# Kernel optimization log

Hardware: AMD Instinct MI355X
Metric: run time of the kernel (lower is better)

The kernel has to match this reference:

```python
import jax, jax.numpy as jnp
import numpy as np

# ---- module hyperparameters (from init_kwargs) ----
DIST = 25
N_IN, N_HID, N_OUT = 16, 128, 2
D_MODEL, D_STATE, D_CONV, EXPAND, HEADDIM = 256, 64, 4, 2, 64
D_INNER = EXPAND * D_MODEL            # 512
NHEADS = D_INNER // HEADDIM           # 8
CONV_DIM = D_INNER + 2 * D_STATE      # 640 (x, B, C share the conv)
D_IN_PROJ = 2 * D_INNER + 2 * D_STATE + NHEADS  # 1160
NUM_CHECK = DIST ** 2 - 1             # 624 (mamba seq len)
NPG = NUM_CHECK + DIST ** 2           # 1249 nodes per graph
BATCH = 64
N_NODES = BATCH * NPG                 # 79936
N_EDGES = N_NODES * 8                 # 639488


def setup_inputs() -> dict:
    key = jax.random.key(0)
    ks = jax.random.split(key, 16)
    w = lambda k, shape, s=0.02: jax.random.normal(k, shape, jnp.float32) * s
    return {
        "node_inputs": jax.random.normal(ks[0], (N_NODES, N_IN), jnp.float32),
        "src_ids": jax.random.randint(ks[1], (N_EDGES,), 0, N_NODES),
        "dst_ids": jax.random.randint(ks[2], (N_EDGES,), 0, N_NODES),
        "W_embed": w(ks[3], (N_IN, D_MODEL)), "b_embed": jnp.zeros((D_MODEL,), jnp.float32),
        "W_in": w(ks[4], (D_MODEL, D_IN_PROJ)), "b_in": jnp.zeros((D_IN_PROJ,), jnp.float32),
        "conv_w": w(ks[5], (CONV_DIM, D_CONV), 0.1), "conv_b": jnp.zeros((CONV_DIM,), jnp.float32),
        "A_log": jnp.log(jnp.arange(1, NHEADS + 1, dtype=jnp.float32)),
        "dt_bias": w(ks[6], (NHEADS,), 0.1),
        "D_skip": jnp.ones((NHEADS,), jnp.float32),
        "norm_w": jnp.ones((D_INNER,), jnp.float32),
        "W_outp": w(ks[7], (D_INNER, D_MODEL)), "b_outp": jnp.zeros((D_MODEL,), jnp.float32),
        "W_proj": w(ks[8], (D_MODEL, N_IN)), "b_proj": jnp.zeros((N_IN,), jnp.float32),
        "W_msg": w(ks[9], (N_IN, N_HID)), "b_msg": jnp.zeros((N_HID,), jnp.float32),
        "W_upd": w(ks[10], (N_IN + N_HID, N_HID)), "b_upd": jnp.zeros((N_HID,), jnp.float32),
        "W_out": w(ks[11], (N_HID, N_OUT)), "b_out": jnp.zeros((N_OUT,), jnp.float32),
    }


def _silu(x):
    return x * jax.nn.sigmoid(x)


def _mamba2(x, W_in, b_in, conv_w, conv_b, A_log, dt_bias, D_skip, norm_w, W_outp, b_outp):
    """Mamba2 block: in_proj -> causal depthwise conv -> selective scan -> gated RMSNorm -> out_proj."""
    Bg, L, _ = x.shape
    zxbcdt = x @ W_in + b_in                       # [Bg, L, 1160]
    z = zxbcdt[..., :D_INNER]                      # gate
    xBC = zxbcdt[..., D_INNER:D_INNER + CONV_DIM]
    dt = zxbcdt[..., D_INNER + CONV_DIM:]          # [Bg, L, H]
    # causal depthwise conv over the seq dim (d_conv taps)
    xp = jnp.pad(xBC, ((0, 0), (D_CONV - 1, 0), (0, 0)))
    xBC = sum(conv_w[:, k] * xp[:, k:k + L, :] for k in range(D_CONV)) + conv_b
    xBC = _silu(xBC)
    xs = xBC[..., :D_INNER].reshape(Bg, L, NHEADS, HEADDIM)
    Bm = xBC[..., D_INNER:D_INNER + D_STATE]       # [Bg, L, N] (ngroups=1)
    Cm = xBC[..., D_INNER + D_STATE:]              # [Bg, L, N]
    dt = jax.nn.softplus(dt + dt_bias)             # [Bg, L, H]
    dA = jnp.exp(dt * (-jnp.exp(A_log)))           # [Bg, L, H]

    def step(h, inp):
        xt, Bt, Ct, dAt, dtt = inp                 # xt [Bg,H,P], Bt/Ct [Bg,N], dAt/dtt [Bg,H]
        h = dAt[..., None, None] * h + dtt[..., None, None] * xt[..., None] * Bt[:, None, None, :]
        yt = jnp.einsum('bhpn,bn->bhp', h, Ct)
        return h, yt

    h0 = jnp.zeros((Bg, NHEADS, HEADDIM, D_STATE), x.dtype)
    seq = (jnp.moveaxis(xs, 1, 0), jnp.moveaxis(Bm, 1, 0), jnp.moveaxis(Cm, 1, 0),
           jnp.moveaxis(dA, 1, 0), jnp.moveaxis(dt, 1, 0))
    _, ys = jax.lax.scan(step, h0, seq)
    ys = jnp.moveaxis(ys, 1, 0) + xs * D_skip[None, None, :, None]   # [Bg, L, H, P]
    y = ys.reshape(Bg, L, D_INNER) * _silu(z)                        # gated
    y = y * jax.lax.rsqrt(jnp.mean(y * y, axis=-1, keepdims=True) + 1e-5) * norm_w
    return y @ W_outp + b_outp


def reference(node_inputs, src_ids, dst_ids, W_embed, b_embed, W_in, b_in, conv_w, conv_b,
              A_log, dt_bias, D_skip, norm_w, W_outp, b_outp, W_proj, b_proj,
              W_msg, b_msg, W_upd, b_upd, W_out, b_out):
    # gather check-node rows: i*nodes_per_graph + j for j < num_check
    idx = (jnp.arange(BATCH)[:, None] * NPG + jnp.arange(NUM_CHECK)[None, :]).reshape(-1)
    chk = node_inputs[idx]                                           # [B*624, 16]
    emb = (chk @ W_embed + b_embed).reshape(BATCH, NUM_CHECK, D_MODEL)
    y = _mamba2(emb, W_in, b_in, conv_w, conv_b, A_log, dt_bias, D_skip, norm_w, W_outp, b_outp)
    proj = y.reshape(-1, D_MODEL) @ W_proj + b_proj                  # [B*624, 16]
    # scatter back into zero tensor at check-node slots
    feat = jnp.zeros((node_inputs.shape[0], N_IN), node_inputs.dtype).at[idx].set(proj)
    # GNN message passing: gather src, transform, scatter-sum into dst, update, readout
    msg = jax.nn.relu(feat[src_ids] @ W_msg + b_msg)                 # [E, n_hidden]
    agg = jax.ops.segment_sum(msg, dst_ids, num_segments=feat.shape[0])
    h = jax.nn.relu(jnp.concatenate([feat, agg], axis=-1) @ W_upd + b_upd)
    return h @ W_out + b_out                                         # [N, n_node_outputs]
```

## Files before the change

### kernel.cpp

```cpp
#include <hip/hip_runtime.h>
#include <math.h>

#define LSEQ 624
#define NPG_C 1249
#define BATCH_C 64
#define NROWS (BATCH_C*LSEQ)
#define N_NODES_C 79936
#define N_EDGES_C 639488
#define DIP 1160
#define DIN 512
#define CDIM 640
#define NH 8
#define HD 64
#define DS 64
#define CAP 96
#define TCH 48
#define NCHK 13
#define HSLOT 2097152

#define OFF_CHK   0
#define OFF_WF    638976
#define OFF_BF    657536
#define OFF_WOP   658944
#define OFF_BOP   667136
#define OFF_XBC   667392
#define OFF_DTV   26226432
#define OFF_EV    26545920
#define OFF_YS    26865408
#define OFF_FEAT  47312640
#define OFF_AGG   48591616
#define OFF_ECUM  (OFF_AGG + 2000000)
#define OFF_BBF   (OFF_AGG + 2400000)
#define OFF_PROJ  (OFF_XBC + 8000000)

typedef __attribute__((ext_vector_type(8))) short bf16x8;
typedef __attribute__((ext_vector_type(4))) float f32x4;

__device__ __forceinline__ float siluf(float x) {
    return x / (1.f + __expf(-x));
}

__device__ __forceinline__ unsigned short f2bf(float f) {
    unsigned int u = __float_as_uint(f);
    u += 0x7fffu + ((u >> 16) & 1u);
    return (unsigned short)(u >> 16);
}
__device__ __forceinline__ float bf2f(unsigned short h) {
    return __uint_as_float(((unsigned int)h) << 16);
}

__device__ __forceinline__ unsigned short* hstp(unsigned short* hst, int c, int b, int head) {
    return hst + (size_t)(c - 1) * HSLOT + (size_t)(b * NH + head) * 4096;
}

__global__ void k_gather(const float* __restrict__ ni, float* __restrict__ chk) {
    int gid = blockIdx.x * 256 + threadIdx.x;
    if (gid >= NROWS * 16) return;
    int row = gid >> 4, k = gid & 15;
    int node = (row / LSEQ) * NPG_C + (row % LSEQ);
    chk[gid] = ni[node * 16 + k];
}

__global__ void k_fusew(const float* __restrict__ We, const float* __restrict__ be,
                        const float* __restrict__ Wi, const float* __restrict__ bi,
                        const float* __restrict__ Wo, const float* __restrict__ bo,
                        const float* __restrict__ Wp, const float* __restrict__ bp,
                        float* __restrict__ Wf, float* __restrict__ bf,
                        float* __restrict__ Wop, float* __restrict__ bop) {
    int id = blockIdx.x * 256 + threadIdx.x;
    if (id < 16 * DIP) {
        int i = id / DIP, j = id % DIP;
        float s = 0.f;
        for (int k = 0; k < 256; k++) s = fmaf(We[i * 256 + k], Wi[k * DIP + j], s);
        Wf[id] = s;
    } else if (id < 16 * DIP + DIP) {
        int j = id - 16 * DIP;
        float s = bi[j];
        for (int k = 0; k < 256; k++) s = fmaf(be[k], Wi[k * DIP + j], s);
        bf[j] = s;
    } else if (id < 16 * DIP + DIP + DIN * 16) {
        int id2 = id - (16 * DIP + DIP);
        int c = id2 >> 4, o = id2 & 15;
        float s = 0.f;
        for (int k = 0; k < 256; k++) s = fmaf(Wo[c * 256 + k], Wp[k * 16 + o], s);
        Wop[id2] = s;
    } else if (id < 16 * DIP + DIP + DIN * 16 + 16) {
        int o = id - (16 * DIP + DIP + DIN * 16);
        float s = bp[o];
        for (int k = 0; k < 256; k++) s = fmaf(bo[k], Wp[k * 16 + o], s);
        bop[o] = s;
    }
}

__global__ __launch_bounds__(320) void k_conv(const float* __restrict__ chk,
        const float* __restrict__ Wf, const float* __restrict__ bf,
        const float* __restrict__ cw, const float* __restrict__ cb,
        float* __restrict__ xBCc, unsigned short* __restrict__ bbf) {
    int c = blockIdx.x * 320 + threadIdx.x;
    int t0 = blockIdx.y * 78;
    int b = blockIdx.z;
    float w[16];
#pragma unroll
    for (int k = 0; k < 16; k++) w[k] = Wf[k * DIP + DIN + c];
    float bfx = bf[DIN + c];
    float k0 = cw[c * 4 + 0], k1 = cw[c * 4 + 1], k2 = cw[c * 4 + 2], k3 = cw[c * 4 + 3];
    float cbv = cb[c];
    const float* crow = chk + (size_t)(b * LSEQ) * 16;
    float* out = xBCc + (size_t)(b * LSEQ) * CDIM + c;
    int isB = (c >= 512 && c < 576);
    unsigned short* bout = bbf + (size_t)(b * LSEQ) * 64 + (c - 512);

    float w0 = 0.f, w1 = 0.f, w2 = 0.f;
#pragma unroll
    for (int d = 3; d >= 1; d--) {
        int tau = t0 - d;
        float s = 0.f;
        if (tau >= 0) {
            s = bfx;
            const float* cr = crow + tau * 16;
#pragma unroll
            for (int k = 0; k < 16; k++) s = fmaf(cr[k], w[k], s);
        }
        if (d == 3) w0 = s; else if (d == 2) w1 = s; else w2 = s;
    }
    for (int t = t0; t < t0 + 78; t++) {
        const float* cr = crow + t * 16;
        float w3 = bfx;
#pragma unroll
        for (int k = 0; k < 16; k++) w3 = fmaf(cr[k], w[k], w3);
        float a = fmaf(k0, w0, fmaf(k1, w1, fmaf(k2, w2, fmaf(k3, w3, cbv))));
        float v = siluf(a);
        out[(size_t)t * CDIM] = v;
        if (isB) bout[(size_t)t * 64] = f2bf(v);
        w0 = w1; w1 = w2; w2 = w3;
    }
}

__global__ __launch_bounds__(256) void k_dte(const float* __restrict__ chk,
        const float* __restrict__ Wf, const float* __restrict__ bf,
        const float* __restrict__ A_log, const float* __restrict__ dt_bias,
        float* __restrict__ dtv, float* __restrict__ ecum) {
    int s = blockIdx.x * 4 + (threadIdx.x >> 6);
    int lane = threadIdx.x & 63;
    int h = s & 7;
    int cb = s >> 3;
    int c = cb % NCHK, b = cb / NCHK;
    int r0 = b * LSEQ + c * TCH;
    float wcol[16];
#pragma unroll
    for (int k = 0; k < 16; k++) wcol[k] = Wf[k * DIP + DIN + CDIM + h];
    float base = bf[DIN + CDIM + h] + dt_bias[h];
    float nA = -__expf(A_log[h]);
    float v = 0.f, sp = 0.f;
    if (lane < TCH) {
        const float* cr = chk + (size_t)(r0 + lane) * 16;
        float acc = base;
#pragma unroll
        for (int k = 0; k < 16; k++) acc = fmaf(cr[k], wcol[k], acc);
        sp = (acc > 20.f) ? acc : log1pf(__expf(acc));
        v = nA * sp;
    }
#pragma unroll
    for (int off = 1; off < 64; off <<= 1) {
        float u = __shfl_up(v, off);
        if (lane >= off) v += u;
    }
    if (lane < TCH) {
        dtv[(size_t)(r0 + lane) * NH + h] = sp;
        ecum[(size_t)(r0 + lane) * NH + h] = v;
    }
}

__global__ __launch_bounds__(256) void k_gmat(const float* __restrict__ xBCc,
        float* __restrict__ Gm) {
    int c = blockIdx.x, b = blockIdx.y;
    int tid = threadIdx.x;
    int bs = b * LSEQ;
    __shared__ __align__(16) float sBC[TCH * 132];
#pragma unroll
    for (int j = 0; j < 6; j++) {
        int g = j * 256 + tid;
        int f = g * 4;
        int t = f >> 7, col = f & 127;
        float4 v = *(const float4*)(xBCc + (size_t)(bs + c * TCH + t) * CDIM + 512 + col);
        *(float4*)&sBC[t * 132 + col] = v;
    }
    __syncthreads();
    int t0 = (tid >> 4) * 3, s0 = (tid & 15) * 3;
    float acc[3][3];
#pragma unroll
    for (int i = 0; i < 3; i++)
#pragma unroll
        for (int j = 0; j < 3; j++) acc[i][j] = 0.f;
    for (int k = 0; k < 64; k++) {
        float c0 = sBC[(t0 + 0) * 132 + 64 + k];
        float c1 = sBC[(t0 + 1) * 132 + 64 + k];
        float c2 = sBC[(t0 + 2) * 132 + 64 + k];
        float b0 = sBC[(s0 + 0) * 132 + k];
        float b1 = sBC[(s0 + 1) * 132 + k];
        float b2 = sBC[(s0 + 2) * 132 + k];
        acc[0][0] = fmaf(c0, b0, acc[0][0]); acc[0][1] = fmaf(c0, b1, acc[0][1]); acc[0][2] = fmaf(c0, b2, acc[0][2]);
        acc[1][0] = fmaf(c1, b0, acc[1][0]); acc[1][1] = fmaf(c1, b1, acc[1][1]); acc[1][2] = fmaf(c1, b2, acc[1][2]);
        acc[2][0] = fmaf(c2, b0, acc[2][0]); acc[2][1] = fmaf(c2, b1, acc[2][1]); acc[2][2] = fmaf(c2, b2, acc[2][2]);
    }
    size_t gb = (size_t)(b * NCHK + c) * (TCH * TCH);
#pragma unroll
    for (int i = 0; i < 3; i++)
#pragma unroll
        for (int j = 0; j < 3; j++)
            Gm[gb + (t0 + i) * TCH + (s0 + j)] = acc[i][j];
}

__global__ __launch_bounds__(256) void k_scarry(const float* __restrict__ xBCc,
        const unsigned short* __restrict__ bbf,
        const float* __restrict__ dtv, const float* __restrict__ ecum,
        unsigned short* __restrict__ hst) {
    int head = blockIdx.x, b = blockIdx.y;
    int tid = threadIdx.x;
    int lane = tid & 63, wv = tid >> 6;
    int bs = b * LSEQ;
    __shared__ unsigned short sXh[64 * 72];
    __shared__ unsigned short sXl[64 * 72];
    __shared__ unsigned short sBn[64 * 72];

    int colL = lane & 15;
    int rbase = (lane >> 4) * 4;
    int kfrag = 8 * (lane >> 4);

    f32x4 acc[4] = { {0,0,0,0}, {0,0,0,0}, {0,0,0,0}, {0,0,0,0} };

    float4 rX[3];
    ushort4 rBu[3];
    float rEc[3], rDt[3], rEcL = 0.f;

#define SC_ISSUE(cc)                                                                \
    {                                                                               \
        int r0i = bs + (cc) * TCH;                                                  \
        _Pragma("unroll")                                                           \
        for (int jj = 0; jj < 3; jj++) {                                            \
            int g = jj * 256 + tid; int t = g >> 4; int col = (g & 15) * 4;         \
            rX[jj] = *(const float4*)(xBCc + (size_t)(r0i + t) * CDIM + head * HD + col); \
            rBu[jj] = *(const ushort4*)(bbf + (size_t)(r0i + t) * 64 + col);        \
            rEc[jj] = ecum[(size_t)(r0i + t) * NH + head];                          \
            rDt[jj] = dtv[(size_t)(r0i + t) * NH + head];                           \
        }                                                                           \
        rEcL = ecum[(size_t)(r0i + TCH - 1) * NH + head];                           \
    }

    {
        int p = tid >> 2, k4 = 48 + (tid & 3) * 4;
        ushort4 z = { 0, 0, 0, 0 };
        *(ushort4*)&sXh[p * 72 + k4] = z;
        *(ushort4*)&sXl[p * 72 + k4] = z;
        *(ushort4*)&sBn[p * 72 + k4] = z;
    }

    SC_ISSUE(0);
    for (int c = 0; c < NCHK; c++) {
        __syncthreads();
        float eL = __expf(rEcL);
#pragma unroll
        for (int jj = 0; jj < 3; jj++) {
            int g = jj * 256 + tid;
            int t = g >> 4, col = (g & 15) * 4;
            float w = __expf(rEcL - rEc[jj]) * rDt[jj];
            float m0 = w * rX[jj].x, m1 = w * rX[jj].y;
            float m2 = w * rX[jj].z, m3 = w * rX[jj].w;
            unsigned short h0 = f2bf(m0), h1 = f2bf(m1), h2 = f2bf(m2), h3 = f2bf(m3);
            sXh[(col + 0) * 72 + t] = h0;
            sXh[(col + 1) * 72 + t] = h1;
            sXh[(col + 2) * 72 + t] = h2;
            sXh[(col + 3) * 72 + t] = h3;
            sXl[(col + 0) * 72 + t] = f2bf(m0 - bf2f(h0));
            sXl[(col + 1) * 72 + t] = f2bf(m1 - bf2f(h1));
            sXl[(col + 2) * 72 + t] = f2bf(m2 - bf2f(h2));
            sXl[(col + 3) * 72 + t] = f2bf(m3 - bf2f(h3));
            sBn[(col + 0) * 72 + t] = rBu[jj].x;
            sBn[(col + 1) * 72 + t] = rBu[jj].y;
            sBn[(col + 2) * 72 + t] = rBu[jj].z;
            sBn[(col + 3) * 72 + t] = rBu[jj].w;
        }
        __syncthreads();
        if (c + 1 < NCHK) SC_ISSUE(c + 1);

        if (c > 0) {
            unsigned short* hp = hstp(hst, c, b, head);
#pragma unroll
            for (int nt = 0; nt < 4; nt++)
#pragma unroll
                for (int r = 0; r < 4; r++)
                    hp[(wv * 16 + rbase + r) * 64 + nt * 16 + colL] = f2bf(acc[nt][r]);
        }
#pragma unroll
        for (int nt = 0; nt < 4; nt++)
#pragma unroll
            for (int r = 0; r < 4; r++)
                acc[nt][r] *= eL;
#pragma unroll
        for (int ks = 0; ks < 64; ks += 32) {
            bf16x8 ah = *(const bf16x8*)&sXh[(wv * 16 + colL) * 72 + ks + kfrag];
            bf16x8 al = *(const bf16x8*)&sXl[(wv * 16 + colL) * 72 + ks + kfrag];
#pragma unroll
            for (int nt = 0; nt < 4; nt++) {
                bf16x8 bb = *(const bf16x8*)&sBn[(nt * 16 + colL) * 72 + ks + kfrag];
                acc[nt] = __builtin_amdgcn_mfma_f32_16x16x32_bf16(ah, bb, acc[nt], 0, 0, 0);
                acc[nt] = __builtin_amdgcn_mfma_f32_16x16x32_bf16(al, bb, acc[nt], 0, 0, 0);
            }
        }
    }
#undef SC_ISSUE
}

__global__ __launch_bounds__(256) void k_intra(float* __restrict__ xBCc,
        const float* __restrict__ Gm, const float* __restrict__ dtv,
        const float* __restrict__ ecum, const float* __restrict__ Dskip,
        const unsigned short* __restrict__ hst) {
    int bid = blockIdx.x;
    int xcd = bid & 7;
    int head = (bid >> 3) & 7;
    int g = (bid >> 6) * 8 + xcd;
    int c = g % NCHK, b = g / NCHK;
    int tid = threadIdx.x;
    int lane = tid & 63;
    int wv = tid >> 6;
    int bs = b * LSEQ;
    int r0 = bs + c * TCH;

    __shared__ __align__(16) unsigned char smraw[35904];
    float* sXf = (float*)(smraw);
    unsigned short* sMh = (unsigned short*)(smraw + 12288);
    unsigned short* sMl = (unsigned short*)(smraw + 19200);
    unsigned short* sCt = (unsigned short*)(smraw + 19200);
    unsigned short* sXh = (unsigned short*)(smraw + 26112);
    unsigned short* sHt = (unsigned short*)(smraw + 26112);
    float* sE  = (float*)(smraw + 35328);
    float* sEx = (float*)(smraw + 35520);
    float* sdt = (float*)(smraw + 35712);

    ushort4 rHu[4];
    if (c > 0) {
        const unsigned short* hp = hstp((unsigned short*)hst, c, b, head);
#pragma unroll
        for (int j = 0; j < 4; j++)
            rHu[j] = *(const ushort4*)(hp + 4 * (j * 256 + tid));
    }

    ushort4 rCu[3];
#pragma unroll
    for (int j = 0; j < 3; j++) {
        int g2 = j * 256 + tid;
        int t = g2 >> 4, col = (g2 & 15) * 4;
        const float* rowp = xBCc + (size_t)(r0 + t) * CDIM;
        float4 xv = *(const float4*)(rowp + head * HD + col);
        *(float4*)&sXf[t * 64 + col] = xv;
        float4 cv = *(const float4*)(rowp + 576 + col);
        ushort4 cu = { f2bf(cv.x), f2bf(cv.y), f2bf(cv.z), f2bf(cv.w) };
        rCu[j] = cu;
    }
    if (tid < TCH) {
        float e = ecum[(size_t)(r0 + tid) * NH + head];
        sE[tid] = e;
        sEx[tid] = __expf(e);
        sdt[tid] = dtv[(size_t)(r0 + tid) * NH + head];
    }
    __syncthreads();

    size_t gb = (size_t)(b * NCHK + c) * (TCH * TCH);
#pragma unroll
    for (int k = 0; k < 9; k++) {
        int id = k * 256 + tid;
        int t = id / TCH, s = id - t * TCH;
        float gv = Gm[gb + id];
        float m = (s <= t) ? __expf(sE[t] - sE[s]) * sdt[s] * gv : 0.f;
        unsigned short mh = f2bf(m);
        sMh[t * 72 + s] = mh;
        sMl[t * 72 + s] = f2bf(m - bf2f(mh));
    }
    for (int w = tid; w < 768; w += 256) {
        int t = w >> 4, s = 48 + (w & 15);
        sMh[t * 72 + s] = 0;
        sMl[t * 72 + s] = 0;
    }
#pragma unroll
    for (int i = 0; i < 3; i++) {
        int w = i * 256 + tid;
        int p = w & 63, k4 = (w >> 6) * 4;
        float v0 = sXf[(k4 + 0) * 64 + p];
        float v1 = sXf[(k4 + 1) * 64 + p];
        float v2 = sXf[(k4 + 2) * 64 + p];
        float v3 = sXf[(k4 + 3) * 64 + p];
        ushort4 hi = { f2bf(v0), f2bf(v1), f2bf(v2), f2bf(v3) };
        *(ushort4*)&sXh[p * 72 + k4] = hi;
    }
    {
        int p = tid >> 2, k4 = 48 + (tid & 3) * 4;
        ushort4 z = { 0, 0, 0, 0 };
        *(ushort4*)&sXh[p * 72 + k4] = z;
    }
    __syncthreads();

    int pt = wv * 16;
    int colL = lane & 15;
    int rbase = (lane >> 4) * 4;
    int kfrag = 8 * (lane >> 4);

    float xo[3][4];
#pragma unroll
    for (int tt = 0; tt < 3; tt++)
#pragma unroll
        for (int r = 0; r < 4; r++)
            xo[tt][r] = sXf[(tt * 16 + rbase + r) * 64 + pt + colL];

    f32x4 acc[3] = { {0,0,0,0}, {0,0,0,0}, {0,0,0,0} };
    f32x4 acc2[3] = { {0,0,0,0}, {0,0,0,0}, {0,0,0,0} };
#pragma unroll
    for (int ks = 0; ks < 64; ks += 32) {
        bf16x8 bh = *(const bf16x8*)&sXh[(pt + colL) * 72 + ks + kfrag];
#pragma unroll
        for (int tt = 0; tt < 3; tt++) {
            bf16x8 ah = *(const bf16x8*)&sMh[(tt * 16 + colL) * 72 + ks + kfrag];
            bf16x8 al = *(const bf16x8*)&sMl[(tt * 16 + colL) * 72 + ks + kfrag];
            acc[tt] = __builtin_amdgcn_mfma_f32_16x16x32_bf16(ah, bh, acc[tt], 0, 0, 0);
            acc[tt] = __builtin_amdgcn_mfma_f32_16x16x32_bf16(al, bh, acc[tt], 0, 0, 0);
        }
    }
    __syncthreads();
#pragma unroll
    for (int j = 0; j < 3; j++) {
        int g2 = j * 256 + tid;
        int t = g2 >> 4, col = (g2 & 15) * 4;
        *(ushort4*)&sCt[t * 72 + col] = rCu[j];
    }
    if (c > 0) {
#pragma unroll
        for (int j = 0; j < 4; j++) {
            int e = 4 * (j * 256 + tid);
            int p = e >> 6, n4 = e & 63;
            *(ushort4*)&sHt[p * 72 + n4] = rHu[j];
        }
    }
    __syncthreads();
    if (c > 0) {
#pragma unroll
        for (int ks = 0; ks < 64; ks += 32) {
            bf16x8 bhh = *(const bf16x8*)&sHt[(pt + colL) * 72 + ks + kfrag];
#pragma unroll
            for (int tt = 0; tt < 3; tt++) {
                bf16x8 ac = *(const bf16x8*)&sCt[(tt * 16 + colL) * 72 + ks + kfrag];
                acc2[tt] = __builtin_amdgcn_mfma_f32_16x16x32_bf16(ac, bhh, acc2[tt], 0, 0, 0);
            }
        }
    }

    float dsk = Dskip[head];
#pragma unroll
    for (int tt = 0; tt < 3; tt++) {
#pragma unroll
        for (int r = 0; r < 4; r++) {
            int trow = tt * 16 + rbase + r;
            float y = fmaf(dsk, xo[tt][r], acc[tt][r]);
            if (c > 0) y = fmaf(sEx[trow], acc2[tt][r], y);
            xBCc[(size_t)(r0 + trow) * CDIM + head * HD + pt + colL] = y;
        }
    }
}

__global__ __launch_bounds__(256) void k_gate(const float* __restrict__ chk,
        const float* __restrict__ Wf, const float* __restrict__ bf,
        const float* __restrict__ ysx, const float* __restrict__ norm_w,
        const float* __restrict__ Wop, const float* __restrict__ bop,
        float* __restrict__ feat) {
    int row0 = blockIdx.x * 8;
    int tid = threadIdx.x;
    __shared__ float sy[2][512];
    __shared__ float sred[2][256];
    __shared__ float swave[2][4];
    int c1 = tid, c2 = tid + 256;
    float wz1[16], wz2[16];
#pragma unroll
    for (int k = 0; k < 16; k++) {
        wz1[k] = Wf[k * DIP + c1];
        wz2[k] = Wf[k * DIP + c2];
    }
    float zb1 = bf[c1], zb2 = bf[c2];
    float nw1 = norm_w[c1], nw2 = norm_w[c2];
    int o = tid & 15, kg = tid >> 4;
    int wid = tid >> 6, lane = tid & 63;

    for (int g2 = 0; g2 < 4; g2++) {
        int rb = row0 + g2 * 2;
        float gn1[2], gn2[2];
#pragma unroll
        for (int r = 0; r < 2; r++) {
            int row = rb + r;
            const float4* cp = (const float4*)(chk + (size_t)row * 16);
            float4 cA = cp[0], cB = cp[1], cC = cp[2], cD = cp[3];
            float cv[16] = {cA.x,cA.y,cA.z,cA.w, cB.x,cB.y,cB.z,cB.w,
                            cC.x,cC.y,cC.z,cC.w, cD.x,cD.y,cD.z,cD.w};
            float z1 = zb1, z2 = zb2;
#pragma unroll
            for (int k = 0; k < 16; k++) {
                z1 = fmaf(cv[k], wz1[k], z1);
                z2 = fmaf(cv[k], wz2[k], z2);
            }
            float y1 = ysx[(size_t)row * CDIM + c1] * siluf(z1);
            float y2 = ysx[(size_t)row * CDIM + c2] * siluf(z2);
            gn1[r] = y1;
            gn2[r] = y2;
            float ss = y1 * y1 + y2 * y2;
#pragma unroll
            for (int off = 32; off >= 1; off >>= 1) ss += __shfl_xor(ss, off);
            if (lane == 0) swave[r][wid] = ss;
        }
        __syncthreads();
#pragma unroll
        for (int r = 0; r < 2; r++) {
            float tot = swave[r][0] + swave[r][1] + swave[r][2] + swave[r][3];
            float scale = 1.f / sqrtf(tot * (1.f / 512.f) + 1e-5f);
            sy[r][c1] = gn1[r] * scale * nw1;
            sy[r][c2] = gn2[r] * scale * nw2;
        }
        __syncthreads();
#pragma unroll
        for (int r = 0; r < 2; r++) {
            float ps = 0.f;
#pragma unroll
            for (int j = 0; j < 32; j++) {
                int k = kg * 32 + j;
                ps = fmaf(sy[r][k], Wop[k * 16 + o], ps);
            }
            sred[r][kg * 16 + o] = ps;
        }
        __syncthreads();
        if (tid < 32) {
            int r = tid >> 4, oo = tid & 15;
            float s = bop[oo];
#pragma unroll
            for (int g = 0; g < 16; g++) s += sred[r][g * 16 + oo];
            int row = rb + r;
            int bb = row / LSEQ, t = row % LSEQ;
            feat[(size_t)(bb * NPG_C + t) * 16 + oo] = s;
        }
    }
}

__global__ void k_scatter(const int* __restrict__ src, const int* __restrict__ dst,
                          int* __restrict__ cnt, int* __restrict__ slots) {
    int e = blockIdx.x * 256 + threadIdx.x;
    if (e >= N_EDGES_C) return;
    int d = dst[e];
    int pos = atomicAdd(&cnt[d], 1);
    if (pos < CAP) slots[(size_t)d * CAP + pos] = src[e];
}

__global__ __launch_bounds__(256) void k_proj(const float* __restrict__ feat,
        const float* __restrict__ Wm, const float* __restrict__ bm,
        unsigned short* __restrict__ p) {
    int tid = threadIdx.x;
    int c = tid & 127, half = tid >> 7;
    float w[16];
#pragma unroll
    for (int k = 0; k < 16; k++) w[k] = Wm[k * 128 + c];
    float bmv = bm[c];
    int base = blockIdx.x * 8;
#pragma unroll
    for (int q = 0; q < 4; q++) {
        int node = base + q * 2 + half;
        const float4* fr = (const float4*)(feat + (size_t)node * 16);
        float4 f0 = fr[0], f1 = fr[1], f2 = fr[2], f3 = fr[3];
        float m = bmv;
        m = fmaf(f0.x, w[0],  m); m = fmaf(f0.y, w[1],  m);
        m = fmaf(f0.z, w[2],  m); m = fmaf(f0.w, w[3],  m);
        m = fmaf(f1.x, w[4],  m); m = fmaf(f1.y, w[5],  m);
        m = fmaf(f1.z, w[6],  m); m = fmaf(f1.w, w[7],  m);
        m = fmaf(f2.x, w[8],  m); m = fmaf(f2.y, w[9],  m);
        m = fmaf(f2.z, w[10], m); m = fmaf(f2.w, w[11], m);
        m = fmaf(f3.x, w[12], m); m = fmaf(f3.y, w[13], m);
        m = fmaf(f3.z, w[14], m); m = fmaf(f3.w, w[15], m);
        p[(size_t)node * 128 + c] = f2bf(fmaxf(m, 0.f));
    }
}

__global__ __launch_bounds__(256) void k_agg2(const int* __restrict__ cnt,
        const int* __restrict__ slots, const unsigned short* __restrict__ p,
        float* __restrict__ agg) {
    int wid = threadIdx.x >> 6, lane = threadIdx.x & 63;
    int esub = lane >> 4, cl = lane & 15;
    int d = blockIdx.x * 4 + wid;
    int deg = cnt[d];
    if (deg > CAP) deg = CAP;
    const int* sl = slots + (size_t)d * CAP;

    float acc[8];
#pragma unroll
    for (int j = 0; j < 8; j++) acc[j] = 0.f;

    int e = esub;
    int s = (e < deg) ? sl[e] : -1;
    while (e < deg) {
        int scur = s;
        int en = e + 4;
        if (en < deg) s = sl[en];
        ushort4 v0, v1;
        {
            const unsigned short* pp = p + (size_t)scur * 128 + cl * 8;
            v0 = *(const ushort4*)(pp);
            v1 = *(const ushort4*)(pp + 4);
        }
        acc[0] += bf2f(v0.x); acc[1] += bf2f(v0.y);
        acc[2] += bf2f(v0.z); acc[3] += bf2f(v0.w);
        acc[4] += bf2f(v1.x); acc[5] += bf2f(v1.y);
        acc[6] += bf2f(v1.z); acc[7] += bf2f(v1.w);
        e = en;
    }
#pragma unroll
    for (int j = 0; j < 8; j++) {
        acc[j] += __shfl_xor(acc[j], 16);
        acc[j] += __shfl_xor(acc[j], 32);
    }
    if (esub == 0) {
        float4 o0 = { acc[0], acc[1], acc[2], acc[3] };
        float4 o1 = { acc[4], acc[5], acc[6], acc[7] };
        float* ap = agg + (size_t)d * 128 + cl * 8;
        *(float4*)(ap) = o0;
        *(float4*)(ap + 4) = o1;
    }
}

#define UNB 32
__global__ __launch_bounds__(256) void k_upd2(const float* __restrict__ feat,
        const float* __restrict__ agg, const float* __restrict__ Wu,
        const float* __restrict__ bu, const float* __restrict__ Wo2,
        const float* __restrict__ bo2, float* __restrict__ out) {
    int g0 = blockIdx.x * UNB;
    int tid = threadIdx.x;
    __shared__ __align__(16) float sin_[UNB][144];
    __shared__ float part[4][8][2];
    for (int w = tid; w < UNB * 144; w += 256) {
        int node = w / 144, k = w - node * 144;
        sin_[node][k] = (k < 16) ? feat[(size_t)(g0 + node) * 16 + k]
                                 : agg[(size_t)(g0 + node) * 128 + (k - 16)];
    }
    __syncthreads();
    int c6 = tid & 63;
    int grp = tid >> 6;
    float acc[8][2];
#pragma unroll
    for (int nn = 0; nn < 8; nn++) { acc[nn][0] = 0.f; acc[nn][1] = 0.f; }

    for (int k0 = 0; k0 < 144; k0 += 4) {
        float wA0 = Wu[(k0 + 0) * 128 + c6], wB0 = Wu[(k0 + 0) * 128 + 64 + c6];
        float wA1 = Wu[(k0 + 1) * 128 + c6], wB1 = Wu[(k0 + 1) * 128 + 64 + c6];
        float wA2 = Wu[(k0 + 2) * 128 + c6], wB2 = Wu[(k0 + 2) * 128 + 64 + c6];
        float wA3 = Wu[(k0 + 3) * 128 + c6], wB3 = Wu[(k0 + 3) * 128 + 64 + c6];
#pragma unroll
        for (int nn = 0; nn < 8; nn++) {
            float4 s4 = *(const float4*)&sin_[grp * 8 + nn][k0];
            acc[nn][0] = fmaf(s4.x, wA0, acc[nn][0]);
            acc[nn][1] = fmaf(s4.x, wB0, acc[nn][1]);
            acc[nn][0] = fmaf(s4.y, wA1, acc[nn][0]);
            acc[nn][1] = fmaf(s4.y, wB1, acc[nn][1]);
            acc[nn][0] = fmaf(s4.z, wA2, acc[nn][0]);
            acc[nn][1] = fmaf(s4.z, wB2, acc[nn][1]);
            acc[nn][0] = fmaf(s4.w, wA3, acc[nn][0]);
            acc[nn][1] = fmaf(s4.w, wB3, acc[nn][1]);
        }
    }

    float buA = bu[c6], buB = bu[64 + c6];
    float2 woA = *(const float2*)&Wo2[c6 * 2];
    float2 woB = *(const float2*)&Wo2[(64 + c6) * 2];
    float p[8][2];
#pragma unroll
    for (int nn = 0; nn < 8; nn++) {
        float h0 = fmaxf(acc[nn][0] + buA, 0.f);
        float h1 = fmaxf(acc[nn][1] + buB, 0.f);
        p[nn][0] = h0 * woA.x + h1 * woB.x;
        p[nn][1] = h0 * woA.y + h1 * woB.y;
    }
#pragma unroll
    for (int off = 1; off < 64; off <<= 1) {
#pragma unroll
        for (int nn = 0; nn < 8; nn++) {
            p[nn][0] += __shfl_xor(p[nn][0], off);
            p[nn][1] += __shfl_xor(p[nn][1], off);
        }
    }
    if ((tid & 63) == 0) {
#pragma unroll
        for (int nn = 0; nn < 8; nn++) {
            part[grp][nn][0] = p[nn][0];
            part[grp][nn][1] = p[nn][1];
        }
    }
    __syncthreads();
    if (tid < 64) {
        int node = tid >> 1, o = tid & 1;
        out[(size_t)(g0 + node) * 2 + o] = part[node >> 3][node & 7][o] + bo2[o];
    }
}

extern "C" void kernel_launch(void* const* d_in, const int* in_sizes, int n_in,
                              void* d_out, int out_size, void* d_ws, size_t ws_size,
                              hipStream_t stream) {
    const float* node_inputs = (const float*)d_in[0];
    const int*   src_ids     = (const int*)d_in[1];
    const int*   dst_ids     = (const int*)d_in[2];
    const float* W_embed     = (const float*)d_in[3];
    const float* b_embed     = (const float*)d_in[4];
    const float* W_in        = (const float*)d_in[5];
    const float* b_in        = (const float*)d_in[6];
    const float* conv_w      = (const float*)d_in[7];
    const float* conv_b      = (const float*)d_in[8];
    const float* A_log       = (const float*)d_in[9];
    const float* dt_bias     = (const float*)d_in[10];
    const float* D_skip      = (const float*)d_in[11];
    const float* norm_w      = (const float*)d_in[12];
    const float* W_outp      = (const float*)d_in[13];
    const float* b_outp      = (const float*)d_in[14];
    const float* W_proj      = (const float*)d_in[15];
    const float* b_proj      = (const float*)d_in[16];
    const float* W_msg       = (const float*)d_in[17];
    const float* b_msg       = (const float*)d_in[18];
    const float* W_upd       = (const float*)d_in[19];
    const float* b_upd       = (const float*)d_in[20];
    const float* W_out       = (const float*)d_in[21];
    const float* b_out       = (const float*)d_in[22];

    float* ws   = (float*)d_ws;
    float* chk  = ws + OFF_CHK;
    float* Wf   = ws + OFF_WF;
    float* bf   = ws + OFF_BF;
    float* Wop  = ws + OFF_WOP;
    float* bop  = ws + OFF_BOP;
    float* xBCc = ws + OFF_XBC;
    float* dtv  = ws + OFF_DTV;
    float* ecum = ws + OFF_ECUM;
    unsigned short* hst = (unsigned short*)(ws + OFF_YS);
    unsigned short* bbf = (unsigned short*)(ws + OFF_BBF);
    float* feat = ws + OFF_FEAT;
    float* agg  = ws + OFF_AGG;
    float* Gm   = ws + OFF_AGG;
    unsigned short* pmsg = (unsigned short*)(ws + OFF_PROJ);
    int*   slots = (int*)(ws + OFF_XBC);
    int*   cnt   = (int*)(ws + OFF_DTV);
    float* out  = (float*)d_out;

    hipMemsetAsync(feat, 0, (size_t)N_NODES_C * 16 * 4, stream);

    k_gather<<<(NROWS * 16 + 255) / 256, 256, 0, stream>>>(node_inputs, chk);
    k_fusew<<<(16 * DIP + DIP + DIN * 16 + 16 + 255) / 256, 256, 0, stream>>>(
        W_embed, b_embed, W_in, b_in, W_outp, b_outp, W_proj, b_proj, Wf, bf, Wop, bop);
    k_conv<<<dim3(2, 8, BATCH_C), 320, 0, stream>>>(chk, Wf, bf, conv_w, conv_b, xBCc, bbf);
    k_dte<<<(BATCH_C * NCHK * NH) / 4, 256, 0, stream>>>(chk, Wf, bf, A_log, dt_bias, dtv, ecum);
    k_gmat<<<dim3(NCHK, BATCH_C), 256, 0, stream>>>(xBCc, Gm);
    k_scarry<<<dim3(NH, BATCH_C), 256, 0, stream>>>(xBCc, bbf, dtv, ecum, hst);
    k_intra<<<NCHK * NH * BATCH_C, 256, 0, stream>>>(xBCc, Gm, dtv, ecum, D_skip, hst);
    k_gate<<<NROWS / 8, 256, 0, stream>>>(chk, Wf, bf, xBCc, norm_w, Wop, bop, feat);
    hipMemsetAsync(cnt, 0, (size_t)N_NODES_C * 4, stream);
    k_scatter<<<(N_EDGES_C + 255) / 256, 256, 0, stream>>>(src_ids, dst_ids, cnt, slots);
    k_proj<<<N_NODES_C / 8, 256, 0, stream>>>(feat, W_msg, b_msg, pmsg);
    k_agg2<<<N_NODES_C / 4, 256, 0, stream>>>(cnt, slots, pmsg, agg);
    k_upd2<<<N_NODES_C / UNB, 256, 0, stream>>>(feat, agg, W_upd, b_upd, W_out, b_out, out);
}
```

Measured before the change: 380.6 us.

## Fuse C·Bᵀ Gram matrix into intra-chunk kernel using bf16 MFMA

Removes the separate k_gmat kernel that computed the per-chunk C·Bᵀ matrix in fp32 and wrote it to global memory. k_intra now computes it itself with bf16 MFMA, taking B from the bf16 copy and C converted to bf16, and keeps the result in shared memory. This saves one launch plus the global write and read of Gm. The trade-offs are less accuracy (single bf16 instead of fp32 FMA), more shared memory per block, and extra syncthreads, while the work is recomputed across the 8 heads.

```diff
diff --git a/kernel.cpp b/kernel.cpp
--- a/kernel.cpp
+++ b/kernel.cpp
@@ -171,46 +171,6 @@
     }
 }
 
-__global__ __launch_bounds__(256) void k_gmat(const float* __restrict__ xBCc,
-        float* __restrict__ Gm) {
-    int c = blockIdx.x, b = blockIdx.y;
-    int tid = threadIdx.x;
-    int bs = b * LSEQ;
-    __shared__ __align__(16) float sBC[TCH * 132];
-#pragma unroll
-    for (int j = 0; j < 6; j++) {
-        int g = j * 256 + tid;
-        int f = g * 4;
-        int t = f >> 7, col = f & 127;
-        float4 v = *(const float4*)(xBCc + (size_t)(bs + c * TCH + t) * CDIM + 512 + col);
-        *(float4*)&sBC[t * 132 + col] = v;
-    }
-    __syncthreads();
-    int t0 = (tid >> 4) * 3, s0 = (tid & 15) * 3;
-    float acc[3][3];
-#pragma unroll
-    for (int i = 0; i < 3; i++)
-#pragma unroll
-        for (int j = 0; j < 3; j++) acc[i][j] = 0.f;
-    for (int k = 0; k < 64; k++) {
-        float c0 = sBC[(t0 + 0) * 132 + 64 + k];
-        float c1 = sBC[(t0 + 1) * 132 + 64 + k];
-        float c2 = sBC[(t0 + 2) * 132 + 64 + k];
-        float b0 = sBC[(s0 + 0) * 132 + k];
-        float b1 = sBC[(s0 + 1) * 132 + k];
-        float b2 = sBC[(s0 + 2) * 132 + k];
-        acc[0][0] = fmaf(c0, b0, acc[0][0]); acc[0][1] = fmaf(c0, b1, acc[0][1]); acc[0][2] = fmaf(c0, b2, acc[0][2]);
-        acc[1][0] = fmaf(c1, b0, acc[1][0]); acc[1][1] = fmaf(c1, b1, acc[1][1]); acc[1][2] = fmaf(c1, b2, acc[1][2]);
-        acc[2][0] = fmaf(c2, b0, acc[2][0]); acc[2][1] = fmaf(c2, b1, acc[2][1]); acc[2][2] = fmaf(c2, b2, acc[2][2]);
-    }
-    size_t gb = (size_t)(b * NCHK + c) * (TCH * TCH);
-#pragma unroll
-    for (int i = 0; i < 3; i++)
-#pragma unroll
-        for (int j = 0; j < 3; j++)
-            Gm[gb + (t0 + i) * TCH + (s0 + j)] = acc[i][j];
-}
-
 __global__ __launch_bounds__(256) void k_scarry(const float* __restrict__ xBCc,
         const unsigned short* __restrict__ bbf,
         const float* __restrict__ dtv, const float* __restrict__ ecum,
@@ -312,9 +272,9 @@
 }
 
 __global__ __launch_bounds__(256) void k_intra(float* __restrict__ xBCc,
-        const float* __restrict__ Gm, const float* __restrict__ dtv,
-        const float* __restrict__ ecum, const float* __restrict__ Dskip,
-        const unsigned short* __restrict__ hst) {
+        const unsigned short* __restrict__ bbf,
+        const float* __restrict__ dtv, const float* __restrict__ ecum,
+        const float* __restrict__ Dskip, const unsigned short* __restrict__ hst) {
     int bid = blockIdx.x;
     int xcd = bid & 7;
     int head = (bid >> 3) & 7;
@@ -326,16 +286,24 @@
     int bs = b * LSEQ;
     int r0 = bs + c * TCH;
 
-    __shared__ __align__(16) unsigned char smraw[35904];
+    __shared__ __align__(16) unsigned char smraw[38208];
+    unsigned short* sCt2 = (unsigned short*)(smraw);
+    unsigned short* sBs  = (unsigned short*)(smraw + 6912);
     float* sXf = (float*)(smraw);
-    unsigned short* sMh = (unsigned short*)(smraw + 12288);
-    unsigned short* sMl = (unsigned short*)(smraw + 19200);
-    unsigned short* sCt = (unsigned short*)(smraw + 19200);
-    unsigned short* sXh = (unsigned short*)(smraw + 26112);
-    unsigned short* sHt = (unsigned short*)(smraw + 26112);
-    float* sE  = (float*)(smraw + 35328);
-    float* sEx = (float*)(smraw + 35520);
-    float* sdt = (float*)(smraw + 35712);
+    float* sG  = (float*)(smraw + 13824);
+    unsigned short* sXh = (unsigned short*)(smraw + 13824);
+    unsigned short* sHt = (unsigned short*)(smraw + 13824);
+    unsigned short* sMh = (unsigned short*)(smraw + 23808);
+    unsigned short* sMl = (unsigned short*)(smraw + 30720);
+    unsigned short* sCt = (unsigned short*)(smraw + 30720);
+    float* sE  = (float*)(smraw + 37632);
+    float* sEx = (float*)(smraw + 37824);
+    float* sdt = (float*)(smraw + 38016);
+
+    int colL = lane & 15;
+    int rbase = (lane >> 4) * 4;
+    int kfrag = 8 * (lane >> 4);
+    int pt = wv * 16;
 
     ushort4 rHu[4];
     if (c > 0) {
@@ -345,17 +313,20 @@
             rHu[j] = *(const ushort4*)(hp + 4 * (j * 256 + tid));
     }
 
+    float4 rXv[3];
     ushort4 rCu[3];
 #pragma unroll
     for (int j = 0; j < 3; j++) {
         int g2 = j * 256 + tid;
         int t = g2 >> 4, col = (g2 & 15) * 4;
         const float* rowp = xBCc + (size_t)(r0 + t) * CDIM;
-        float4 xv = *(const float4*)(rowp + head * HD + col);
-        *(float4*)&sXf[t * 64 + col] = xv;
+        rXv[j] = *(const float4*)(rowp + head * HD + col);
         float4 cv = *(const float4*)(rowp + 576 + col);
         ushort4 cu = { f2bf(cv.x), f2bf(cv.y), f2bf(cv.z), f2bf(cv.w) };
         rCu[j] = cu;
+        ushort4 bu = *(const ushort4*)(bbf + (size_t)(r0 + t) * 64 + col);
+        *(ushort4*)&sCt2[t * 72 + col] = cu;
+        *(ushort4*)&sBs[t * 72 + col] = bu;
     }
     if (tid < TCH) {
         float e = ecum[(size_t)(r0 + tid) * NH + head];
@@ -365,12 +336,36 @@
     }
     __syncthreads();
 
-    size_t gb = (size_t)(b * NCHK + c) * (TCH * TCH);
+#pragma unroll
+    for (int slot = 0; slot < 3; slot++) {
+        int idx = wv + slot * 4;
+        if (idx < 9) {
+            int tt = idx / 3, ss = idx - tt * 3;
+            f32x4 a = { 0.f, 0.f, 0.f, 0.f };
+#pragma unroll
+            for (int ks = 0; ks < 64; ks += 32) {
+                bf16x8 ca = *(const bf16x8*)&sCt2[(tt * 16 + colL) * 72 + ks + kfrag];
+                bf16x8 bb = *(const bf16x8*)&sBs[(ss * 16 + colL) * 72 + ks + kfrag];
+                a = __builtin_amdgcn_mfma_f32_16x16x32_bf16(ca, bb, a, 0, 0, 0);
+            }
+#pragma unroll
+            for (int r = 0; r < 4; r++)
+                sG[(tt * 16 + rbase + r) * 52 + ss * 16 + colL] = a[r];
+        }
+    }
+    __syncthreads();
+
+#pragma unroll
+    for (int j = 0; j < 3; j++) {
+        int g2 = j * 256 + tid;
+        int t = g2 >> 4, col = (g2 & 15) * 4;
+        *(float4*)&sXf[t * 64 + col] = rXv[j];
+    }
 #pragma unroll
     for (int k = 0; k < 9; k++) {
         int id = k * 256 + tid;
         int t = id / TCH, s = id - t * TCH;
-        float gv = Gm[gb + id];
+        float gv = sG[t * 52 + s];
         float m = (s <= t) ? __expf(sE[t] - sE[s]) * sdt[s] * gv : 0.f;
         unsigned short mh = f2bf(m);
         sMh[t * 72 + s] = mh;
@@ -381,6 +376,8 @@
         sMh[t * 72 + s] = 0;
         sMl[t * 72 + s] = 0;
     }
+    __syncthreads();
+
 #pragma unroll
     for (int i = 0; i < 3; i++) {
         int w = i * 256 + tid;
@@ -397,19 +394,13 @@
         ushort4 z = { 0, 0, 0, 0 };
         *(ushort4*)&sXh[p * 72 + k4] = z;
     }
-    __syncthreads();
-
-    int pt = wv * 16;
-    int colL = lane & 15;
-    int rbase = (lane >> 4) * 4;
-    int kfrag = 8 * (lane >> 4);
-
     float xo[3][4];
 #pragma unroll
     for (int tt = 0; tt < 3; tt++)
 #pragma unroll
         for (int r = 0; r < 4; r++)
             xo[tt][r] = sXf[(tt * 16 + rbase + r) * 64 + pt + colL];
+    __syncthreads();
 
     f32x4 acc[3] = { {0,0,0,0}, {0,0,0,0}, {0,0,0,0} };
     f32x4 acc2[3] = { {0,0,0,0}, {0,0,0,0}, {0,0,0,0} };
@@ -740,7 +731,6 @@
     unsigned short* bbf = (unsigned short*)(ws + OFF_BBF);
     float* feat = ws + OFF_FEAT;
     float* agg  = ws + OFF_AGG;
-    float* Gm   = ws + OFF_AGG;
     unsigned short* pmsg = (unsigned short*)(ws + OFF_PROJ);
     int*   slots = (int*)(ws + OFF_XBC);
     int*   cnt   = (int*)(ws + OFF_DTV);
@@ -753,9 +743,8 @@
         W_embed, b_embed, W_in, b_in, W_outp, b_outp, W_proj, b_proj, Wf, bf, Wop, bop);
     k_conv<<<dim3(2, 8, BATCH_C), 320, 0, stream>>>(chk, Wf, bf, conv_w, conv_b, xBCc, bbf);
     k_dte<<<(BATCH_C * NCHK * NH) / 4, 256, 0, stream>>>(chk, Wf, bf, A_log, dt_bias, dtv, ecum);
-    k_gmat<<<dim3(NCHK, BATCH_C), 256, 0, stream>>>(xBCc, Gm);
     k_scarry<<<dim3(NH, BATCH_C), 256, 0, stream>>>(xBCc, bbf, dtv, ecum, hst);
-    k_intra<<<NCHK * NH * BATCH_C, 256, 0, stream>>>(xBCc, Gm, dtv, ecum, D_skip, hst);
+    k_intra<<<NCHK * NH * BATCH_C, 256, 0, stream>>>(xBCc, bbf, dtv, ecum, D_skip, hst);
     k_gate<<<NROWS / 8, 256, 0, stream>>>(chk, Wf, bf, xBCc, norm_w, Wop, bop, feat);
     hipMemsetAsync(cnt, 0, (size_t)N_NODES_C * 4, stream);
     k_scatter<<<(N_EDGES_C + 255) / 256, 256, 0, stream>>>(src_ids, dst_ids, cnt, slots);
```

Result: no change. 374.4 us (-1.6%).
